# Kernel tuning notes

Hardware: AMD Instinct MI355X
Metric: run time of the kernel (lower is better)

The kernel has to match this reference:

```python
import jax, jax.numpy as jnp
import numpy as np

D_MODEL = 1024
NUM_HEADS = 16
HEAD_DIM = D_MODEL // NUM_HEADS


def setup_inputs() -> dict:
    key = jax.random.key(0)
    ks = jax.random.split(key, 5)
    B, S, D_IN = 2, 2048, 1024
    x = jax.random.normal(ks[0], (B, S, D_IN), dtype=jnp.float32)
    std = 0.02
    wq = jax.random.normal(ks[1], (D_MODEL, D_IN), dtype=jnp.float32) * std
    wk = jax.random.normal(ks[2], (D_MODEL, D_IN), dtype=jnp.float32) * std
    wv = jax.random.normal(ks[3], (D_MODEL, D_IN), dtype=jnp.float32) * std
    wo = jax.random.normal(ks[4], (D_IN, D_MODEL), dtype=jnp.float32) * std
    return {"x": x, "wq": wq, "wk": wk, "wv": wv, "wo": wo}


def _mha(x, wq, wk, wv, wo):
    B, S, _ = x.shape
    H, Dh = NUM_HEADS, HEAD_DIM
    # projections: Linear applies x @ W.T with W of shape [out, in]
    q = (x @ wq.T).reshape(B, S, H, Dh).transpose(0, 2, 1, 3)  # [B,H,S,Dh]
    k = (x @ wk.T).reshape(B, S, H, Dh).transpose(0, 2, 1, 3)
    v = (x @ wv.T).reshape(B, S, H, Dh).transpose(0, 2, 1, 3)
    scores = jnp.einsum('bhqd,bhkd->bhqk', q, k) / jnp.sqrt(jnp.float32(Dh))
    causal = jnp.tril(jnp.ones((S, S), dtype=bool))  # True where attended
    scores = jnp.where(causal, scores, -jnp.inf)
    attn = jax.nn.softmax(scores, axis=-1)
    out = jnp.einsum('bhqk,bhkd->bhqd', attn, v)  # [B,H,S,Dh]
    out = out.transpose(0, 2, 1, 3).reshape(B, S, H * Dh)
    return out @ wo.T


def reference(x, wq, wk, wv, wo):
    return _mha(x, wq, wk, wv, wo)
```

## Files before the change

kernel.cpp:

```cpp
#include <hip/hip_runtime.h>
#include <hip/hip_bf16.h>
#include <stdint.h>

using bf16 = __hip_bfloat16;
typedef __attribute__((ext_vector_type(4))) short shorts4;
typedef __attribute__((ext_vector_type(8))) short short8;
typedef __attribute__((ext_vector_type(4))) float floatx4;
typedef __attribute__((ext_vector_type(16))) float floatx16;
typedef __attribute__((ext_vector_type(4))) unsigned int uintx4;

constexpr int BATCH = 2;
constexpr int SEQ   = 2048;
constexpr int NH    = 16;
constexpr int DH    = 64;
constexpr int DM    = 1024;
constexpr int MROWS = BATCH * SEQ;
constexpr int OUTN  = MROWS * DM;
constexpr int WN    = DM * DM;

__device__ inline short bfbits(float x) {
    bf16 h = __float2bfloat16(x);
    return __builtin_bit_cast(short, h);
}

__device__ inline unsigned pack2(float a, float b) {
    return (unsigned)(unsigned short)bfbits(a) |
           ((unsigned)(unsigned short)bfbits(b) << 16);
}

__device__ inline void async16(bf16* lds, const bf16* g) {
    __builtin_amdgcn_global_load_lds(
        (const __attribute__((address_space(1))) unsigned int*)g,
        (__attribute__((address_space(3))) unsigned int*)lds, 16, 0, 0);
}

__device__ inline void cvt8(const float* src, bf16* dst) {
    float4 f0 = *(const float4*)(src);
    float4 f1 = *(const float4*)(src + 4);
    short8 o;
    o[0] = bfbits(f0.x); o[1] = bfbits(f0.y); o[2] = bfbits(f0.z); o[3] = bfbits(f0.w);
    o[4] = bfbits(f1.x); o[5] = bfbits(f1.y); o[6] = bfbits(f1.z); o[7] = bfbits(f1.w);
    *(short8*)(dst) = o;
}

__global__ __launch_bounds__(256)
void cvt_all(const float* __restrict__ x,  const float* __restrict__ wq,
             const float* __restrict__ wk, const float* __restrict__ wv,
             const float* __restrict__ wo, bf16* __restrict__ dst,
             bf16* __restrict__ wob)
{
    const size_t i = ((size_t)blockIdx.x * 256 + threadIdx.x) * 8;
    if (i < (size_t)OUTN + 3 * WN) {
        const float* src; size_t off;
        if (i < (size_t)OUTN)               { src = x;  off = i; }
        else if (i < (size_t)OUTN + WN)     { src = wq; off = i - OUTN; }
        else if (i < (size_t)OUTN + 2 * WN) { src = wk; off = i - OUTN - WN; }
        else                                { src = wv; off = i - OUTN - 2 * (size_t)WN; }
        cvt8(src + off, dst + i);
    } else {
        const size_t off = i - OUTN - 3 * (size_t)WN;
        cvt8(wo + off, wob + off);
    }
}

__global__ __launch_bounds__(256)
void cvt_inputs(const float* __restrict__ x,  const float* __restrict__ wq,
                const float* __restrict__ wk, const float* __restrict__ wv,
                bf16* __restrict__ dst)
{
    const size_t i = ((size_t)blockIdx.x * 256 + threadIdx.x) * 8;
    const float* src; size_t off;
    if (i < (size_t)OUTN)               { src = x;  off = i; }
    else if (i < (size_t)OUTN + WN)     { src = wq; off = i - OUTN; }
    else if (i < (size_t)OUTN + 2 * WN) { src = wk; off = i - OUTN - WN; }
    else                                { src = wv; off = i - OUTN - 2 * (size_t)WN; }
    cvt8(src + off, dst + i);
}

__global__ __launch_bounds__(256)
void cvt_wo(const float* __restrict__ wo, bf16* __restrict__ dst)
{
    const size_t i = ((size_t)blockIdx.x * 256 + threadIdx.x) * 8;
    cvt8(wo + i, dst + i);
}

template<int MODE, int NT>
__global__ __launch_bounds__(256)
void gemm_mfma(const bf16* __restrict__ A,
               const bf16* __restrict__ W0, const bf16* __restrict__ W1,
               const bf16* __restrict__ W2,
               bf16* __restrict__ C0, bf16* __restrict__ C1, bf16* __restrict__ C2,
               float* __restrict__ F)
{
    constexpr int NJ = NT / 32;
    __shared__ __align__(16) bf16 As[128 * 32];
    __shared__ __align__(16) bf16 Ws[NT * 32];

    const int t    = threadIdx.x;
    const int wave = t >> 6;
    const int lane = t & 63;
    const int quad = lane >> 4;
    const int l16  = lane & 15;
    const int m0 = blockIdx.y * 128;
    const int n0 = blockIdx.x * NT;
    const int wr = (wave >> 1) * 64;
    const int wc = (wave & 1) * (NT / 2);

    const int z = (MODE == 0) ? blockIdx.z : 0;
    const bf16* W = (z == 0) ? W0 : ((z == 1) ? W1 : W2);

    const int c    = t;
    bf16* lA0 = As + c * 8;          bf16* lA1 = As + c * 8 + 2048;
    bf16* lW0 = Ws + c * 8;          bf16* lW1 = Ws + c * 8 + 2048;
    const int ar0 = m0 + (c >> 2),  ar1 = m0 + 64 + (c >> 2);
    const int nr0 = n0 + (c >> 2),  nr1 = n0 + 64 + (c >> 2);
    const int kc  = (c & 3) * 8;

    floatx4 acc[4][NJ] = {};

    for (int k0 = 0; k0 < DM; k0 += 32) {
        const bf16* gA0 = A + (size_t)ar0 * DM + k0 + kc;
        const bf16* gA1 = A + (size_t)ar1 * DM + k0 + kc;
        const bf16* gW0 = W + (size_t)nr0 * DM + k0 + kc;
        const bf16* gW1 = W + (size_t)nr1 * DM + k0 + kc;

        __syncthreads();
        async16(lA0, gA0);
        async16(lA1, gA1);
        async16(lW0, gW0);
        if (NT == 128) async16(lW1, gW1);
        __syncthreads();

        short8 af[4], wf[NJ];
        #pragma unroll
        for (int i = 0; i < 4; i++)
            af[i] = *(const short8*)(As + (wr + i * 16 + l16) * 32 + quad * 8);
        #pragma unroll
        for (int j = 0; j < NJ; j++)
            wf[j] = *(const short8*)(Ws + (wc + j * 16 + l16) * 32 + quad * 8);
        #pragma unroll
        for (int i = 0; i < 4; i++)
            #pragma unroll
            for (int j = 0; j < NJ; j++)
                acc[i][j] = __builtin_amdgcn_mfma_f32_16x16x32_bf16(af[i], wf[j], acc[i][j], 0, 0, 0);
    }

    #pragma unroll
    for (int i = 0; i < 4; i++) {
        #pragma unroll
        for (int j = 0; j < NJ; j++) {
            if (MODE == 0 && z == 2) {
                const int s0 = m0 + wr + i * 16 + quad * 4;
                const int gn = n0 + wc + j * 16 + l16;
                const int b = s0 >> 11, sr = s0 & (SEQ - 1);
                const int h = gn >> 6,  d = gn & (DH - 1);
                shorts4 pv;
                #pragma unroll
                for (int r = 0; r < 4; r++) pv[r] = bfbits(acc[i][j][r]);
                *(shorts4*)(C2 + (((size_t)(b * NH + h)) * DH + d) * SEQ + sr) = pv;
            } else {
                #pragma unroll
                for (int r = 0; r < 4; r++) {
                    const int gm = m0 + wr + i * 16 + quad * 4 + r;
                    const int gn = n0 + wc + j * 16 + l16;
                    if (MODE == 1) {
                        F[(size_t)gm * DM + gn] = acc[i][j][r];
                    } else {
                        float av = acc[i][j][r];
                        if (z == 0) av *= 0.18033688f;
                        bf16* dst = (z == 0) ? C0 : C1;
                        dst[(size_t)gm * DM + gn] = __float2bfloat16(av);
                    }
                }
            }
        }
    }
}

__global__ __launch_bounds__(256)
void attn_flash(bf16* __restrict__ Q, const bf16* __restrict__ K,
                const bf16* __restrict__ Vt)
{
    __shared__ __align__(16) bf16 smem[16384];
    bf16* Ks = smem;
    bf16* Vs = smem + 8192;

    const int t    = threadIdx.x;
    const int wave = t >> 6;
    const int lane = t & 63;
    const int hi   = lane >> 5;
    const int l32  = lane & 31;

    const int h  = blockIdx.y;
    const int b  = blockIdx.z;
    const int qt = (blockIdx.x + 5 * h + 8 * b) & 15;
    const int q0 = qt * 128;
    const int hc = h * DH;
    const size_t rowb = (size_t)b * SEQ;
    const size_t bhv  = ((size_t)(b * NH + h)) * SEQ * DH;

    const int qrow = q0 + wave * 32;
    const int qg   = qrow + l32;

    short8 qf[4];
    #pragma unroll
    for (int s = 0; s < 4; s++)
        qf[s] = *(const short8*)(Q + (rowb + qg) * DM + hc + s * 16 + hi * 8);

    floatx16 oacc[2] = {};
    float lsum = 0.f;

    for (int k0 = 0; k0 < q0 + 128; k0 += 128) {
        __syncthreads();
        #pragma unroll
        for (int p = 0; p < 4; p++) {
            const int ck = p * 256 + t;
            const int kr = ck >> 3;
            const int kg = (ck & 7) ^ (kr & 7);
            async16(Ks + ck * 8, K + (rowb + k0 + kr) * DM + hc + kg * 8);
            const int vr = ck >> 4;
            const int vg = (ck & 15) ^ (vr & 15);
            async16(Vs + ck * 8, Vt + bhv + (size_t)vr * SEQ + k0 + vg * 8);
        }
        __syncthreads();

        #pragma unroll
        for (int c64 = 0; c64 < 128; c64 += 64) {
            const int kb0 = k0 + c64;
            if (kb0 > qrow + 31) continue;

            #pragma unroll
            for (int kt = 0; kt < 2; kt++) {
                const int kb = kb0 + kt * 32;
                if (kb > qrow + 31) continue;

                const int krow = c64 + kt * 32 + l32;
                floatx16 sc = {};
                #pragma unroll
                for (int s = 0; s < 4; s++) {
                    const int g = (s * 2 + hi) ^ (krow & 7);
                    short8 kf = *(const short8*)(Ks + krow * 64 + g * 8);
                    sc = __builtin_amdgcn_mfma_f32_32x32x16_bf16(kf, qf[s], sc, 0, 0, 0);
                }

                if (kb + 31 > qrow) {
                    #pragma unroll
                    for (int r = 0; r < 16; r++) {
                        const int key = kb + (r & 3) + 8 * (r >> 2) + 4 * hi;
                        sc[r] = (key <= qg) ? sc[r] : -1e30f;
                    }
                }

                #pragma unroll
                for (int r = 0; r < 16; r++) {
                    const float p = __builtin_amdgcn_exp2f(sc[r]);
                    sc[r] = p;
                    lsum += p;
                }

                unsigned d[4][2];
                #pragma unroll
                for (int g = 0; g < 4; g++) {
                    d[g][0] = pack2(sc[4 * g + 0], sc[4 * g + 1]);
                    d[g][1] = pack2(sc[4 * g + 2], sc[4 * g + 3]);
                }

                #pragma unroll
                for (int h16 = 0; h16 < 2; h16++) {
                    const unsigned a0 = d[h16 * 2][0],     a1 = d[h16 * 2][1];
                    const unsigned b0 = d[h16 * 2 + 1][0], b1 = d[h16 * 2 + 1][1];
                    const unsigned mine0 = hi ? b0 : a0, mine1 = hi ? b1 : a1;
                    const unsigned give0 = hi ? a0 : b0, give1 = hi ? a1 : b1;
                    const unsigned r0 = (unsigned)__shfl_xor((int)give0, 32, 64);
                    const unsigned r1 = (unsigned)__shfl_xor((int)give1, 32, 64);
                    uintx4 pw;
                    pw[0] = hi ? r0 : mine0;
                    pw[1] = hi ? r1 : mine1;
                    pw[2] = hi ? mine0 : r0;
                    pw[3] = hi ? mine1 : r1;
                    short8 pb = __builtin_bit_cast(short8, pw);

                    const int Gbase = (c64 >> 3) + kt * 4 + h16 * 2 + hi;
                    #pragma unroll
                    for (int tile = 0; tile < 2; tile++) {
                        const int vrow = tile * 32 + l32;
                        const int vg = Gbase ^ (vrow & 15);
                        short8 vf = *(const short8*)(Vs + vrow * 128 + vg * 8);
                        oacc[tile] = __builtin_amdgcn_mfma_f32_32x32x16_bf16(vf, pb, oacc[tile], 0, 0, 0);
                    }
                }
            }
        }
    }

    lsum += __shfl_xor(lsum, 32, 64);
    const float invl = 1.0f / lsum;

    __syncthreads();
    bf16* T = smem + wave * (32 * 72);
    #pragma unroll
    for (int tile = 0; tile < 2; tile++)
        #pragma unroll
        for (int rq = 0; rq < 4; rq++) {
            shorts4 v4;
            #pragma unroll
            for (int s = 0; s < 4; s++) v4[s] = bfbits(oacc[tile][rq * 4 + s] * invl);
            *(shorts4*)(T + l32 * 72 + tile * 32 + rq * 8 + hi * 4) = v4;
        }
    asm volatile("s_waitcnt lgkmcnt(0)" ::: "memory");
    #pragma unroll
    for (int p = 0; p < 4; p++) {
        const int rq = (lane >> 3) + p * 8;
        const int dd = (lane & 7) * 8;
        short8 v8 = *(const short8*)(T + rq * 72 + dd);
        *(short8*)(Q + (rowb + qrow + rq) * DM + hc + dd) = v8;
    }
}

extern "C" void kernel_launch(void* const* d_in, const int* in_sizes, int n_in,
                              void* d_out, int out_size, void* d_ws, size_t ws_size,
                              hipStream_t stream)
{
    const float* x  = (const float*)d_in[0];
    const float* wq = (const float*)d_in[1];
    const float* wk = (const float*)d_in[2];
    const float* wv = (const float*)d_in[3];
    const float* wo = (const float*)d_in[4];
    float* out = (float*)d_out;

    bf16* qb = (bf16*)d_ws;
    bf16* kb = qb + (size_t)OUTN;
    bf16* vb = kb + (size_t)OUTN;

    bf16* xb  = (bf16*)d_out;
    bf16* wqb = xb + (size_t)OUTN;
    bf16* wkb = wqb + WN;
    bf16* wvb = wkb + WN;

    const bool wsBig = ws_size >= (size_t)(3 * (size_t)OUTN + WN) * sizeof(bf16);

    if (wsBig) {
        bf16* wob = vb + (size_t)OUTN;
        cvt_all<<<(OUTN + 4 * WN) / (8 * 256), 256, 0, stream>>>(
            x, wq, wk, wv, wo, xb, wob);
        gemm_mfma<0, 128><<<dim3(DM / 128, MROWS / 128, 3), dim3(256), 0, stream>>>(
            xb, wqb, wkb, wvb, qb, kb, vb, nullptr);
        attn_flash<<<dim3(SEQ / 128, NH, BATCH), dim3(256), 0, stream>>>(qb, kb, vb);
        gemm_mfma<1, 64><<<dim3(DM / 64, MROWS / 128, 1), dim3(256), 0, stream>>>(
            qb, wob, nullptr, nullptr, nullptr, nullptr, nullptr, out);
    } else {
        cvt_inputs<<<(OUTN + 3 * WN) / (8 * 256), 256, 0, stream>>>(x, wq, wk, wv, xb);
        gemm_mfma<0, 128><<<dim3(DM / 128, MROWS / 128, 3), dim3(256), 0, stream>>>(
            xb, wqb, wkb, wvb, qb, kb, vb, nullptr);
        attn_flash<<<dim3(SEQ / 128, NH, BATCH), dim3(256), 0, stream>>>(qb, kb, vb);
        bf16* wob = kb;
        cvt_wo<<<WN / (8 * 256), 256, 0, stream>>>(wo, wob);
        gemm_mfma<1, 64><<<dim3(DM / 64, MROWS / 128, 1), dim3(256), 0, stream>>>(
            qb, wob, nullptr, nullptr, nullptr, nullptr, nullptr, out);
    }
}
```

Baseline: 191.3 us.

## Split attention keys across two wave groups with double-buffered K/V tiles

The attention kernel moves from 256 to 512 threads. Two groups of four waves each process half of every 128-key tile for the same query rows, and their partial output accumulators and row sums are merged through shared memory at the end. K/V tiles are double-buffered so the next tile's async load overlaps compute on the current one. This raises parallelism per block and hides load latency, at the cost of twice the LDS (64KB), a merge step, and possible lower occupancy from register limits under launch_bounds(512,4).

```diff
diff --git a/kernel.cpp b/kernel.cpp
--- a/kernel.cpp
+++ b/kernel.cpp
@@ -177,13 +177,11 @@
     }
 }
 
-__global__ __launch_bounds__(256)
+__global__ __launch_bounds__(512, 4)
 void attn_flash(bf16* __restrict__ Q, const bf16* __restrict__ K,
                 const bf16* __restrict__ Vt)
 {
-    __shared__ __align__(16) bf16 smem[16384];
-    bf16* Ks = smem;
-    bf16* Vs = smem + 8192;
+    __shared__ __align__(16) bf16 smem[32768];
 
     const int t    = threadIdx.x;
     const int wave = t >> 6;
@@ -199,8 +197,10 @@
     const size_t rowb = (size_t)b * SEQ;
     const size_t bhv  = ((size_t)(b * NH + h)) * SEQ * DH;
 
-    const int qrow = q0 + wave * 32;
-    const int qg   = qrow + l32;
+    const int qw    = wave & 3;
+    const int khalf = wave >> 2;
+    const int qrow  = q0 + qw * 32;
+    const int qg    = qrow + l32;
 
     short8 qf[4];
     #pragma unroll
@@ -210,31 +210,42 @@
     floatx16 oacc[2] = {};
     float lsum = 0.f;
 
-    for (int k0 = 0; k0 < q0 + 128; k0 += 128) {
-        __syncthreads();
-        #pragma unroll
-        for (int p = 0; p < 4; p++) {
-            const int ck = p * 256 + t;
+    const int T = q0 / 128 + 1;
+
+    auto stage = [&](int tt, int bb) {
+        bf16* Kb = smem + bb * 16384;
+        bf16* Vb = Kb + 8192;
+        const int k0 = tt * 128;
+        #pragma unroll
+        for (int p = 0; p < 2; p++) {
+            const int ck = p * 512 + t;
             const int kr = ck >> 3;
             const int kg = (ck & 7) ^ (kr & 7);
-            async16(Ks + ck * 8, K + (rowb + k0 + kr) * DM + hc + kg * 8);
+            async16(Kb + ck * 8, K + (rowb + k0 + kr) * DM + hc + kg * 8);
             const int vr = ck >> 4;
             const int vg = (ck & 15) ^ (vr & 15);
-            async16(Vs + ck * 8, Vt + bhv + (size_t)vr * SEQ + k0 + vg * 8);
+            async16(Vb + ck * 8, Vt + bhv + (size_t)vr * SEQ + k0 + vg * 8);
         }
-        __syncthreads();
-
-        #pragma unroll
-        for (int c64 = 0; c64 < 128; c64 += 64) {
-            const int kb0 = k0 + c64;
-            if (kb0 > qrow + 31) continue;
-
+    };
+
+    stage(0, 0);
+    __syncthreads();
+
+    for (int tt = 0; tt < T; ++tt) {
+        const int cur = tt & 1;
+        if (tt + 1 < T) stage(tt + 1, cur ^ 1);
+
+        const bf16* Ks = smem + cur * 16384;
+        const bf16* Vs = Ks + 8192;
+        const int kbase = tt * 128 + khalf * 64;
+
+        if (kbase <= qrow + 31) {
             #pragma unroll
             for (int kt = 0; kt < 2; kt++) {
-                const int kb = kb0 + kt * 32;
+                const int kb = kbase + kt * 32;
                 if (kb > qrow + 31) continue;
 
-                const int krow = c64 + kt * 32 + l32;
+                const int krow = khalf * 64 + kt * 32 + l32;
                 floatx16 sc = {};
                 #pragma unroll
                 for (int s = 0; s < 4; s++) {
@@ -280,7 +291,7 @@
                     pw[3] = hi ? mine1 : r1;
                     short8 pb = __builtin_bit_cast(short8, pw);
 
-                    const int Gbase = (c64 >> 3) + kt * 4 + h16 * 2 + hi;
+                    const int Gbase = khalf * 8 + kt * 4 + h16 * 2 + hi;
                     #pragma unroll
                     for (int tile = 0; tile < 2; tile++) {
                         const int vrow = tile * 32 + l32;
@@ -291,29 +302,54 @@
                 }
             }
         }
+        __syncthreads();
     }
 
     lsum += __shfl_xor(lsum, 32, 64);
-    const float invl = 1.0f / lsum;
-
+
+    float* dmp = (float*)smem;
+    float* lP  = dmp + 4 * 32 * 65;
+    if (wave >= 4) {
+        const int p = wave - 4;
+        #pragma unroll
+        for (int tile = 0; tile < 2; tile++)
+            #pragma unroll
+            for (int r = 0; r < 16; r++) {
+                const int d = tile * 32 + (r & 3) + 8 * (r >> 2) + 4 * hi;
+                dmp[(p * 32 + l32) * 65 + d] = oacc[tile][r];
+            }
+        if (!hi) lP[p * 32 + l32] = lsum;
+    }
     __syncthreads();
-    bf16* T = smem + wave * (32 * 72);
-    #pragma unroll
-    for (int tile = 0; tile < 2; tile++)
-        #pragma unroll
-        for (int rq = 0; rq < 4; rq++) {
-            shorts4 v4;
+
+    if (wave < 4) {
+        const int p = wave;
+        lsum += lP[p * 32 + l32];
+        const float invl = 1.0f / lsum;
+
+        bf16* T8 = smem + 16896 + wave * (32 * 72);
+        #pragma unroll
+        for (int tile = 0; tile < 2; tile++)
             #pragma unroll
-            for (int s = 0; s < 4; s++) v4[s] = bfbits(oacc[tile][rq * 4 + s] * invl);
-            *(shorts4*)(T + l32 * 72 + tile * 32 + rq * 8 + hi * 4) = v4;
+            for (int rq = 0; rq < 4; rq++) {
+                shorts4 v4;
+                #pragma unroll
+                for (int s = 0; s < 4; s++) {
+                    const int r = rq * 4 + s;
+                    const int d = tile * 32 + (r & 3) + 8 * (r >> 2) + 4 * hi;
+                    const float comb = oacc[tile][r] + dmp[(p * 32 + l32) * 65 + d];
+                    v4[s] = bfbits(comb * invl);
+                }
+                *(shorts4*)(T8 + l32 * 72 + tile * 32 + rq * 8 + hi * 4) = v4;
+            }
+        asm volatile("s_waitcnt lgkmcnt(0)" ::: "memory");
+        #pragma unroll
+        for (int p2 = 0; p2 < 4; p2++) {
+            const int rq = (lane >> 3) + p2 * 8;
+            const int dd = (lane & 7) * 8;
+            short8 v8 = *(const short8*)(T8 + rq * 72 + dd);
+            *(short8*)(Q + (rowb + qrow + rq) * DM + hc + dd) = v8;
         }
-    asm volatile("s_waitcnt lgkmcnt(0)" ::: "memory");
-    #pragma unroll
-    for (int p = 0; p < 4; p++) {
-        const int rq = (lane >> 3) + p * 8;
-        const int dd = (lane & 7) * 8;
-        short8 v8 = *(const short8*)(T + rq * 72 + dd);
-        *(short8*)(Q + (rowb + qrow + rq) * DM + hc + dd) = v8;
     }
 }
 
@@ -345,14 +381,14 @@
             x, wq, wk, wv, wo, xb, wob);
         gemm_mfma<0, 128><<<dim3(DM / 128, MROWS / 128, 3), dim3(256), 0, stream>>>(
             xb, wqb, wkb, wvb, qb, kb, vb, nullptr);
-        attn_flash<<<dim3(SEQ / 128, NH, BATCH), dim3(256), 0, stream>>>(qb, kb, vb);
+        attn_flash<<<dim3(SEQ / 128, NH, BATCH), dim3(512), 0, stream>>>(qb, kb, vb);
         gemm_mfma<1, 64><<<dim3(DM / 64, MROWS / 128, 1), dim3(256), 0, stream>>>(
             qb, wob, nullptr, nullptr, nullptr, nullptr, nullptr, out);
     } else {
         cvt_inputs<<<(OUTN + 3 * WN) / (8 * 256), 256, 0, stream>>>(x, wq, wk, wv, xb);
         gemm_mfma<0, 128><<<dim3(DM / 128, MROWS / 128, 3), dim3(256), 0, stream>>>(
             xb, wqb, wkb, wvb, qb, kb, vb, nullptr);
-        attn_flash<<<dim3(SEQ / 128, NH, BATCH), dim3(256), 0, stream>>>(qb, kb, vb);
+        attn_flash<<<dim3(SEQ / 128, NH, BATCH), dim3(512), 0, stream>>>(qb, kb, vb);
         bf16* wob = kb;
         cvt_wo<<<WN / (8 * 256), 256, 0, stream>>>(wo, wob);
         gemm_mfma<1, 64><<<dim3(DM / 64, MROWS / 128, 1), dim3(256), 0, stream>>>(
```

Result: faster. 173.3 us (-9.4%).
